# Kernel tuning notes

Hardware: AMD Instinct MI355X
Metric: run time of the kernel (lower is better)

## Reference

```python
import jax, jax.numpy as jnp
import numpy as np

N_COARSE = 262145   # GMGN self.n
K_LEVELS = 5        # self.k
M_NBR = 9           # self.m
HID = 2048          # hidden_channels


def _build_grid():
    # replicates GMGN.init_toep_kernel (mtype='toep_mg')
    n_fine = 2 * (N_COARSE - 1) + 1          # 524289
    x = np.linspace(-1.0, 1.0, n_fine)
    x_lst, idx_lst = [], []
    for _ in range(K_LEVELS):
        n = x.shape[0]
        idx = np.arange((n - 1) // 2 - M_NBR + 1, (n - 1) // 2 + M_NBR)[1::2]  # m-1 center pts
        idx_lst.append(idx)
        x_lst.append(x[idx])
        x = x[::2]                            # injection1d
    x_lst.append(x)                           # coarse grid
    xs = np.concatenate(x_lst)[:, None].astype(np.float32)   # (N_eval, 1)
    nbrs = np.stack(idx_lst[::-1]).astype(np.int64)          # (k, m-1), coarse->fine
    return xs, nbrs


def setup_inputs() -> dict:
    key = jax.random.key(0)
    xs_np, nbrs_np = _build_grid()
    dims = [1, HID, HID, HID, HID, 1]
    inp = {"xs": jnp.asarray(xs_np), "nbrs": jnp.asarray(nbrs_np), "k": K_LEVELS, "m": M_NBR}
    ks = jax.random.split(key, 10)
    for j in range(5):
        bd = 1.0 / np.sqrt(dims[j])           # nn.Linear default init range
        inp[f"w{j}"] = jax.random.uniform(ks[2 * j], (dims[j], dims[j + 1]), jnp.float32, -bd, bd)
        inp[f"b{j}"] = jax.random.uniform(ks[2 * j + 1], (dims[j + 1],), jnp.float32, -bd, bd)
    return inp


def _interp1d(a):
    # linear prolongation: (n,) -> (2n-1,); even slots copy, odd slots average
    out = jnp.zeros((2 * a.shape[0] - 1,), a.dtype)
    out = out.at[0::2].set(a)
    return out.at[1::2].set(0.5 * (a[:-1] + a[1:]))


def _forward(xs, Ws, bs, nbrs, k, m):
    h = xs
    for W, b in zip(Ws, bs):
        h = jax.nn.relu(h @ W + b)            # MLP appends relu after every Linear (incl. last)
    Amg = h[:, 0]                             # (N_eval,) pointwise kernel values
    band = m - 1
    Abands = [Amg[band * i: band * (i + 1)] for i in range(k)][::-1]
    Ah = Amg[band * k:]                       # coarse kernel, length (n0-1)/2^k + 1
    for i in range(k):
        Ah = _interp1d(Ah)                    # upsample one level
        Ah = Ah.at[nbrs[i]].set(Abands[i])    # overwrite center band with exact MLP evals
    return Ah[None, None]                     # (1, 1, 2*(n-1)+1)


def reference(xs, w0, b0, w1, b1, w2, b2, w3, b3, w4, b4, nbrs, k, m):
    return _forward(xs, (w0, w1, w2, w3, w4), (b0, b1, b2, b3, b4), nbrs, k, m)
```

## Files before the change

### kernel.cpp

```cpp
#include <hip/hip_runtime.h>
#include <stdint.h>

#define HID    2048
#define MPTS   16425
#define MTILES 129
#define NTIL   16
#define KTIL   64
#define BIMG   5120

typedef float    f32x4 __attribute__((ext_vector_type(4)));
typedef _Float16 f16x8 __attribute__((ext_vector_type(8)));


__global__ void pack_w16(const float* __restrict__ w1,
                         const float* __restrict__ w2,
                         const float* __restrict__ w3,
                         _Float16* __restrict__ wp) {
    const int kt = blockIdx.x, nt = blockIdx.y, L = blockIdx.z;
    const float* W = (L == 0) ? w1 : ((L == 1) ? w2 : w3);
    __shared__ float tl[128 * 33];
    const int tid = threadIdx.x;
    const int k  = tid >> 3;
    const int nc = (tid & 7) * 16;
    const float* src = W + (size_t)(kt * 32 + k) * HID + nt * 128 + nc;
    #pragma unroll
    for (int j = 0; j < 16; ++j) tl[(nc + j) * 33 + k] = src[j];
    __syncthreads();
    const size_t base = (size_t)(L * 1024 + nt * 64 + kt) * BIMG;
    for (int e = tid; e < BIMG; e += 256) {
        int n = e / 40, kk = e - n * 40;
        wp[base + e] = (kk < 32) ? (_Float16)tl[n * 33 + kk] : (_Float16)0.f;
    }
}

__global__ void layer0p(const float* __restrict__ xs,
                        const float* __restrict__ w0,
                        const float* __restrict__ b0,
                        _Float16* __restrict__ Ahg,
                        _Float16* __restrict__ Alg, int row0) {
    const int r = blockIdx.x;
    const int grow = row0 + r;
    const int j0 = threadIdx.x * 8;
    const float x = (grow < MPTS) ? xs[grow] : 0.f;
    f16x8 h, l;
    #pragma unroll
    for (int q = 0; q < 8; ++q) {
        float v = x * w0[j0 + q] + b0[j0 + q];
        v = v > 0.f ? v : 0.f;
        _Float16 hs = (_Float16)v;
        h[q] = hs;
        l[q] = (_Float16)(v - (float)hs);
    }
    const int t = r >> 7, rowgrp = (r >> 4) & 7, lidx = r & 15;
    const int kt = j0 >> 5, quad = (j0 >> 3) & 3;
    const size_t dst = ((size_t)(t * 64 + kt) << 12) + rowgrp * 512 + quad * 128 + lidx * 8;
    *(f16x8*)(Ahg + dst) = h;
    *(f16x8*)(Alg + dst) = l;
}

__launch_bounds__(256, 3)
__global__ void gemm_hl(const _Float16* __restrict__ Ahg,
                        const _Float16* __restrict__ Alg,
                        const _Float16* __restrict__ wp,
                        const float* __restrict__ bias,
                        _Float16* __restrict__ Chg,
                        _Float16* __restrict__ Clg,
                        int layer, int write_lo) {
    __shared__ _Float16 Bs[2][BIMG];

    const int tid  = threadIdx.x;
    const int lane = tid & 63;
    const int wave = tid >> 6;
    const int quad = lane >> 4;
    const int lidx = lane & 15;

    const int nwg = (int)(gridDim.x * gridDim.y);
    const int L   = (int)(blockIdx.y * gridDim.x + blockIdx.x);
    const int F   = (L & 7) * (nwg >> 3) + (L >> 3);
    const int nt  = F & 15;
    const int mt  = F >> 4;

    const int mbase = (wave >> 1) * 64;
    const int nbase = (wave & 1) * 64;

    const char* gW = (const char*)(wp + (size_t)(layer * 1024 + nt * 64) * BIMG);

    const size_t abase = ((size_t)(mt * 64) << 12) + (size_t)(mbase >> 4) * 512 + (size_t)lane * 8;
    const _Float16* aH = Ahg + abase;
    const _Float16* aL = Alg + abase;

    f32x4 acc[4][4];
    #pragma unroll
    for (int i = 0; i < 4; ++i)
        #pragma unroll
        for (int j = 0; j < 4; ++j) acc[i][j] = (f32x4)0.f;

#define PF_B(KT, BUF) do {                                                            \
    const char* nW_ = gW + (size_t)(KT) * (BIMG * 2);                                 \
    char* dW_ = (char*)&Bs[BUF][0];                                                   \
    for (int t = wave; t < 10; t += 4) {                                              \
        __builtin_amdgcn_global_load_lds(                                             \
            (const __attribute__((address_space(1))) unsigned int*)(nW_ + t * 1024 + lane * 16), \
            (__attribute__((address_space(3))) unsigned int*)(dW_ + t * 1024), 16, 0, 0); \
    }                                                                                 \
} while (0)

#define LD_A(KT, H, Lo) do {                                                          \
    const size_t ak_ = (size_t)(KT) << 12;                                            \
    _Pragma("unroll")                                                                 \
    for (int mm = 0; mm < 4; ++mm) {                                                  \
        H[mm]  = *(const f16x8*)(aH + ak_ + mm * 512);                                \
        Lo[mm] = *(const f16x8*)(aL + ak_ + mm * 512);                                \
    }                                                                                 \
} while (0)

#define STEP(KT, BUF, CH, CL, DO_PF, NH, NL, DO_A) do {                               \
    if (DO_PF) PF_B((KT) + 1, (BUF) ^ 1);                                             \
    if (DO_A)  LD_A((KT) + 1, NH, NL);                                                \
    f16x8 bfr_[4];                                                                    \
    _Pragma("unroll")                                                                 \
    for (int nn = 0; nn < 4; ++nn) {                                                  \
        int r_ = nbase + nn * 16 + lidx;                                              \
        bfr_[nn] = *(const f16x8*)(&Bs[BUF][r_ * 40 + quad * 8]);                     \
    }                                                                                 \
    _Pragma("unroll")                                                                 \
    for (int mm = 0; mm < 4; ++mm)                                                    \
        _Pragma("unroll")                                                             \
        for (int nn = 0; nn < 4; ++nn) {                                              \
            acc[mm][nn] = __builtin_amdgcn_mfma_f32_16x16x32_f16(CH[mm], bfr_[nn], acc[mm][nn], 0, 0, 0); \
            acc[mm][nn] = __builtin_amdgcn_mfma_f32_16x16x32_f16(CL[mm], bfr_[nn], acc[mm][nn], 0, 0, 0); \
        }                                                                             \
    __syncthreads();                                                                  \
} while (0)

    f16x8 cah[4], cal[4], nah[4], nal[4];

    PF_B(0, 0);
    LD_A(0, cah, cal);
    __syncthreads();

    for (int kt2 = 0; kt2 < 31; ++kt2) {
        STEP(2 * kt2,     0, cah, cal, 1, nah, nal, 1);
        STEP(2 * kt2 + 1, 1, nah, nal, 1, cah, cal, 1);
    }
    STEP(62, 0, cah, cal, 1, nah, nal, 1);
    STEP(63, 1, nah, nal, 0, cah, cal, 0);

#undef STEP
#undef LD_A
#undef PF_B

    #pragma unroll
    for (int nn = 0; nn < 4; ++nn) {
        const int col = nt * 128 + nbase + nn * 16 + lidx;
        const float bv = bias[col];
        const int kt2 = col >> 5, quad2 = (col >> 3) & 3, j2 = col & 7;
        const size_t cb = ((size_t)(mt * 64 + kt2) << 12) + quad2 * 128 + j2;
        #pragma unroll
        for (int mm = 0; mm < 4; ++mm) {
            const int rowg = (mbase >> 4) + mm;
            #pragma unroll
            for (int r = 0; r < 4; ++r) {
                const int lidx2 = quad * 4 + r;
                float v = acc[mm][nn][r] + bv;
                v = v > 0.f ? v : 0.f;
                _Float16 hs = (_Float16)v;
                const size_t idx = cb + rowg * 512 + lidx2 * 8;
                Chg[idx] = hs;
                if (write_lo) Clg[idx] = (_Float16)(v - (float)hs);
            }
        }
    }
}

__global__ void layer4p(const _Float16* __restrict__ Ahg,
                        const float* __restrict__ w4,
                        const float* __restrict__ b4,
                        float* __restrict__ Amg, int row0) {
    __shared__ float ps[256];
    const int mt = blockIdx.x;
    const int t = threadIdx.x;
    const int row = t & 127, half = t >> 7;
    const int rowgrp = row >> 4, lidx = row & 15;
    const size_t base = ((size_t)(mt * 64) << 12) + rowgrp * 512 + lidx * 8;
    float s = 0.f;
    for (int kt = half * 32; kt < half * 32 + 32; ++kt) {
        const _Float16* ph = Ahg + base + ((size_t)kt << 12);
        const float* wv = w4 + kt * 32;
        #pragma unroll
        for (int quad = 0; quad < 4; ++quad) {
            f16x8 hv = *(const f16x8*)(ph + quad * 128);
            #pragma unroll
            for (int j = 0; j < 8; ++j)
                s += (float)hv[j] * wv[quad * 8 + j];
        }
    }
    ps[t] = s;
    __syncthreads();
    if (t < 128) {
        const int grow = row0 + mt * 128 + t;
        if (grow < MPTS) {
            float v = ps[t] + ps[t + 128] + b4[0];
            Amg[grow] = v > 0.f ? v : 0.f;
        }
    }
}

__global__ void layer0f(const float* __restrict__ xs, const float* __restrict__ w0,
                        const float* __restrict__ b0, float* __restrict__ A, int row0) {
    const int r = blockIdx.x;
    const int j = threadIdx.x * 8;
    const float x = (row0 + r < MPTS) ? xs[row0 + r] : 0.f;
    float* out = A + (size_t)r * HID + j;
    #pragma unroll
    for (int q = 0; q < 8; ++q) {
        float v = x * w0[j + q] + b0[j + q];
        out[q] = v > 0.f ? v : 0.f;
    }
}

__launch_bounds__(256)
__global__ void gemm_valu(const float* __restrict__ A, const float* __restrict__ W,
                          const float* __restrict__ bias, float* __restrict__ C) {
    __shared__ float As[16][132];
    __shared__ float Ws[16][132];
    const int tid = threadIdx.x;
    const int tx = tid & 15, ty = tid >> 4;
    const int n0 = blockIdx.x * 128;
    const int m0 = blockIdx.y * 128;
    const int am = tid & 127, ak = (tid >> 7) * 8;
    const int wn = (tid & 15) * 8, wk = tid >> 4;
    const float* aptr = A + (size_t)(m0 + am) * HID + ak;
    const float* wptr = W + (size_t)wk * HID + n0 + wn;
    float acc[8][8];
    #pragma unroll
    for (int i = 0; i < 8; ++i)
        #pragma unroll
        for (int j = 0; j < 8; ++j) acc[i][j] = 0.f;
    for (int k0 = 0; k0 < HID; k0 += 16) {
        f32x4 a0 = *(const f32x4*)(aptr + k0);
        f32x4 a1 = *(const f32x4*)(aptr + k0 + 4);
        f32x4 w0v = *(const f32x4*)(wptr + (size_t)k0 * HID);
        f32x4 w1v = *(const f32x4*)(wptr + (size_t)k0 * HID + 4);
        __syncthreads();
        As[ak + 0][am] = a0[0]; As[ak + 1][am] = a0[1];
        As[ak + 2][am] = a0[2]; As[ak + 3][am] = a0[3];
        As[ak + 4][am] = a1[0]; As[ak + 5][am] = a1[1];
        As[ak + 6][am] = a1[2]; As[ak + 7][am] = a1[3];
        *(f32x4*)&Ws[wk][wn]     = w0v;
        *(f32x4*)&Ws[wk][wn + 4] = w1v;
        __syncthreads();
        #pragma unroll
        for (int kk = 0; kk < 16; ++kk) {
            f32x4 av0 = *(const f32x4*)&As[kk][ty * 8];
            f32x4 av1 = *(const f32x4*)&As[kk][ty * 8 + 4];
            f32x4 bv0 = *(const f32x4*)&Ws[kk][tx * 8];
            f32x4 bv1 = *(const f32x4*)&Ws[kk][tx * 8 + 4];
            float a[8] = {av0[0], av0[1], av0[2], av0[3], av1[0], av1[1], av1[2], av1[3]};
            float b[8] = {bv0[0], bv0[1], bv0[2], bv0[3], bv1[0], bv1[1], bv1[2], bv1[3]};
            #pragma unroll
            for (int i = 0; i < 8; ++i)
                #pragma unroll
                for (int j = 0; j < 8; ++j) acc[i][j] += a[i] * b[j];
        }
    }
    #pragma unroll
    for (int i = 0; i < 8; ++i) {
        const int m = m0 + ty * 8 + i;
        #pragma unroll
        for (int jc = 0; jc < 2; ++jc) {
            const int n = n0 + tx * 8 + jc * 4;
            f32x4 v4;
            #pragma unroll
            for (int q = 0; q < 4; ++q) {
                float v = acc[i][jc * 4 + q] + bias[n + q];
                v4[q] = v > 0.f ? v : 0.f;
            }
            *(f32x4*)(C + (size_t)m * HID + n) = v4;
        }
    }
}

__global__ void layer4f(const float* __restrict__ A, const float* __restrict__ w4,
                        const float* __restrict__ b4, float* __restrict__ Amg, int row0) {
    const int lane = threadIdx.x & 63;
    const int wave = threadIdx.x >> 6;
    const int r    = blockIdx.x * 4 + wave;
    if (row0 + r >= MPTS) return;
    const float* ap = A + (size_t)r * HID;
    float s = 0.f;
    #pragma unroll
    for (int c = 0; c < 8; ++c) {
        const int col = c * 256 + lane * 4;
        f32x4 av = *(const f32x4*)(ap + col);
        f32x4 wv = *(const f32x4*)(w4 + col);
        s += av[0] * wv[0] + av[1] * wv[1] + av[2] * wv[2] + av[3] * wv[3];
    }
    #pragma unroll
    for (int off = 32; off; off >>= 1) s += __shfl_down(s, off);
    if (lane == 0) {
        float v = s + b4[0];
        Amg[row0 + r] = v > 0.f ? v : 0.f;
    }
}

__global__ void mg_level(const float* __restrict__ in, float* __restrict__ outf,
                         const int* __restrict__ nbrs_base, int level,
                         const float* __restrict__ band, int n_out) {
    const int j = blockIdx.x * 256 + threadIdx.x;
    if (j >= n_out) return;
    float v;
    if (j & 1) v = 0.5f * (in[j >> 1] + in[(j >> 1) + 1]);
    else       v = in[j >> 1];
    const int stride =
        (nbrs_base[1] == 0 && nbrs_base[3] == 0 && nbrs_base[5] == 0) ? 2 : 1;
    #pragma unroll
    for (int t = 0; t < 8; ++t) {
        const int idx = nbrs_base[(level * 8 + t) * stride];
        if (j == idx) v = band[t];
    }
    outf[j] = v;
}

extern "C" void kernel_launch(void* const* d_in, const int* in_sizes, int n_in,
                              void* d_out, int out_size, void* d_ws, size_t ws_size,
                              hipStream_t stream) {
    int iXS=0, iNB=1, iW0=4, iB0=5, iW1=6, iB1=7, iW2=8, iB2=9,
        iW3=10, iB3=11, iW4=12, iB4=13;
    if (n_in >= 14) {
        if (in_sizes[0] == HID) {
            iB0=0; iB1=1; iB2=2; iB3=3; iB4=4; iNB=7;
            iW0=8; iW1=9; iW2=10; iW3=11; iW4=12; iXS=13;
        } else if (!(in_sizes[1] == 40 || in_sizes[1] == 80)) {
            iXS=0; iW0=1; iB0=2; iW1=3; iB1=4; iW2=5; iB2=6;
            iW3=7; iB3=8; iW4=9; iB4=10; iNB=11;
        }
    }
    const float* xs = (const float*)d_in[iXS];
    const int* nbrs = (const int*)d_in[iNB];
    const float* w0 = (const float*)d_in[iW0];
    const float* b0 = (const float*)d_in[iB0];
    const float* w1 = (const float*)d_in[iW1];
    const float* b1 = (const float*)d_in[iB1];
    const float* w2 = (const float*)d_in[iW2];
    const float* b2 = (const float*)d_in[iB2];
    const float* w3 = (const float*)d_in[iW3];
    const float* b3 = (const float*)d_in[iB3];
    const float* w4 = (const float*)d_in[iW4];
    const float* b4 = (const float*)d_in[iB4];

    char* ws = (char*)d_ws;
    const size_t szAmg = 66048;
    const size_t szAh1 = 524544;
    const size_t szAh2 = 1048832;
    float* Amg = (float*)(ws);
    float* ahA = (float*)(ws + szAmg);
    float* ahB = (float*)(ws + szAmg + szAh1);
    const size_t casc_end = szAmg + szAh1 + szAh2;
    const size_t szW    = (size_t)3 * 1024 * BIMG * 2;
    const size_t per_tile = 2ull * 128 * HID * 4;

    const int use_mfma = (ws_size >= casc_end + szW + per_tile) ? 1 : 0;

    _Float16* wp = (_Float16*)(ws + casc_end);
    const size_t buf_start = use_mfma ? (casc_end + szW) : casc_end;

    size_t avail = ws_size - buf_start;
    int CT = (int)(avail / per_tile);
    if (CT < 1) CT = 1;
    if (CT > 96) CT = 96;

    if (use_mfma) {
        const size_t half = (size_t)CT * 128 * HID;
        _Float16* bAh = (_Float16*)(ws + buf_start);
        _Float16* bAl = bAh + half;
        _Float16* bBh = bAh + 2 * half;
        _Float16* bBl = bAh + 3 * half;

        pack_w16<<<dim3(KTIL, NTIL, 3), 256, 0, stream>>>(w1, w2, w3, wp);

        for (int t0 = 0; t0 < MTILES; t0 += CT) {
            int tiles = (MTILES - t0 < CT) ? (MTILES - t0) : CT;
            int row0 = t0 * 128;
            layer0p<<<dim3(tiles * 128), 256, 0, stream>>>(xs, w0, b0, bAh, bAl, row0);
            dim3 ggrid(NTIL, tiles);
            gemm_hl<<<ggrid, 256, 0, stream>>>(bAh, bAl, wp, b1, bBh, bBl, 0, 1);
            gemm_hl<<<ggrid, 256, 0, stream>>>(bBh, bBl, wp, b2, bAh, bAl, 1, 1);
            gemm_hl<<<ggrid, 256, 0, stream>>>(bAh, bAl, wp, b3, bBh, bBl, 2, 0);
            layer4p<<<dim3(tiles), 256, 0, stream>>>(bBh, w4, b4, Amg, row0);
        }
    } else {
        float* bufA = (float*)(ws + buf_start);
        float* bufB = (float*)(ws + buf_start + (size_t)CT * 128 * HID * 4);
        for (int t0 = 0; t0 < MTILES; t0 += CT) {
            int tiles = (MTILES - t0 < CT) ? (MTILES - t0) : CT;
            int row0 = t0 * 128;
            layer0f<<<dim3(tiles * 128), 256, 0, stream>>>(xs, w0, b0, bufA, row0);
            dim3 ggrid(NTIL, tiles);
            gemm_valu<<<ggrid, 256, 0, stream>>>(bufA, w1, b1, bufB);
            gemm_valu<<<ggrid, 256, 0, stream>>>(bufB, w2, b2, bufA);
            gemm_valu<<<ggrid, 256, 0, stream>>>(bufA, w3, b3, bufB);
            layer4f<<<dim3(tiles * 32), 256, 0, stream>>>(bufB, w4, b4, Amg, row0);
        }
    }

    const float* cur = Amg + 40;
    float* dsts[5] = {ahA, ahB, ahA, ahB, (float*)d_out};
    int n = 16385;
    for (int i = 0; i < 5; ++i) {
        int n_out = 2 * n - 1;
        mg_level<<<dim3((n_out + 255) / 256), 256, 0, stream>>>(
            cur, dsts[i], nbrs, i, Amg + 8 * (4 - i), n_out);
        cur = dsts[i];
        n = n_out;
    }
    (void)out_size;
}
```

Before: 1.045 ms.

## Process two K-tiles per barrier with four LDS buffers in GEMM

Expands the shared-memory B staging from two to four buffers and restructures the K loop into super-steps that each cover two K-tiles, prefetching the next pair while computing the current one. This halves the number of __syncthreads barriers per tile and gives the asynchronous global-to-LDS loads more time to land. The cost is doubled LDS usage per block (about 40KB), which may limit the three-blocks-per-CU occupancy target and add register pressure.

```diff
diff --git a/kernel.cpp b/kernel.cpp
--- a/kernel.cpp
+++ b/kernel.cpp
@@ -66,7 +66,7 @@
                         _Float16* __restrict__ Chg,
                         _Float16* __restrict__ Clg,
                         int layer, int write_lo) {
-    __shared__ _Float16 Bs[2][BIMG];
+    __shared__ _Float16 Bs[4][BIMG];
 
     const int tid  = threadIdx.x;
     const int lane = tid & 63;
@@ -114,39 +114,54 @@
     }                                                                                 \
 } while (0)
 
-#define STEP(KT, BUF, CH, CL, DO_PF, NH, NL, DO_A) do {                               \
-    if (DO_PF) PF_B((KT) + 1, (BUF) ^ 1);                                             \
-    if (DO_A)  LD_A((KT) + 1, NH, NL);                                                \
-    f16x8 bfr_[4];                                                                    \
+#define LD_B(BUF, BF) do {                                                            \
     _Pragma("unroll")                                                                 \
     for (int nn = 0; nn < 4; ++nn) {                                                  \
         int r_ = nbase + nn * 16 + lidx;                                              \
-        bfr_[nn] = *(const f16x8*)(&Bs[BUF][r_ * 40 + quad * 8]);                     \
+        BF[nn] = *(const f16x8*)(&Bs[BUF][r_ * 40 + quad * 8]);                       \
     }                                                                                 \
+} while (0)
+
+#define MFMA32(AH, AL, BF) do {                                                       \
     _Pragma("unroll")                                                                 \
     for (int mm = 0; mm < 4; ++mm)                                                    \
         _Pragma("unroll")                                                             \
         for (int nn = 0; nn < 4; ++nn) {                                              \
-            acc[mm][nn] = __builtin_amdgcn_mfma_f32_16x16x32_f16(CH[mm], bfr_[nn], acc[mm][nn], 0, 0, 0); \
-            acc[mm][nn] = __builtin_amdgcn_mfma_f32_16x16x32_f16(CL[mm], bfr_[nn], acc[mm][nn], 0, 0, 0); \
+            acc[mm][nn] = __builtin_amdgcn_mfma_f32_16x16x32_f16(AH[mm], BF[nn], acc[mm][nn], 0, 0, 0); \
+            acc[mm][nn] = __builtin_amdgcn_mfma_f32_16x16x32_f16(AL[mm], BF[nn], acc[mm][nn], 0, 0, 0); \
         }                                                                             \
+} while (0)
+
+#define SUPER(S, P, DO_PF, DO_A2) do {                                                \
+    f16x8 bfr0_[4];                                                                   \
+    LD_B(2 * (P), bfr0_);                                                             \
+    if (DO_PF) { PF_B(2 * (S) + 2, 2 * ((P) ^ 1)); PF_B(2 * (S) + 3, 2 * ((P) ^ 1) + 1); } \
+    LD_A(2 * (S) + 1, nah, nal);                                                      \
+    MFMA32(cah, cal, bfr0_);                                                          \
+    f16x8 bfr1_[4];                                                                   \
+    LD_B(2 * (P) + 1, bfr1_);                                                         \
+    if (DO_A2) LD_A(2 * (S) + 2, cah, cal);                                           \
+    MFMA32(nah, nal, bfr1_);                                                          \
     __syncthreads();                                                                  \
 } while (0)
 
     f16x8 cah[4], cal[4], nah[4], nal[4];
 
     PF_B(0, 0);
+    PF_B(1, 1);
     LD_A(0, cah, cal);
     __syncthreads();
 
-    for (int kt2 = 0; kt2 < 31; ++kt2) {
-        STEP(2 * kt2,     0, cah, cal, 1, nah, nal, 1);
-        STEP(2 * kt2 + 1, 1, nah, nal, 1, cah, cal, 1);
-    }
-    STEP(62, 0, cah, cal, 1, nah, nal, 1);
-    STEP(63, 1, nah, nal, 0, cah, cal, 0);
-
-#undef STEP
+    for (int ss = 0; ss < 15; ++ss) {
+        SUPER(2 * ss,     0, 1, 1);
+        SUPER(2 * ss + 1, 1, 1, 1);
+    }
+    SUPER(30, 0, 1, 1);
+    SUPER(31, 1, 0, 0);
+
+#undef SUPER
+#undef MFMA32
+#undef LD_B
 #undef LD_A
 #undef PF_B
 
```

After: 1.031 ms. About the same (-1.3%).
